# Performance work log

Hardware: AMD Instinct MI355X
Metric: run time of the kernel (lower is better)

## Reference

```python
import jax, jax.numpy as jnp
import numpy as np

N_NODES = 50000
N_EDGES = 800000
D = 128          # d_model
N_LAYER = 4
N_GRAPHS = 128
N_IDS = 256      # nn.Embedding(256, d_model)


def setup_inputs() -> dict:
    key = jax.random.key(0)
    ks = jax.random.split(key, 10)
    s = 0.02
    return {
        "position_feature": jax.random.normal(ks[0], (N_NODES, 3), dtype=jnp.float32),
        "id_feature": jax.random.randint(ks[1], (N_NODES,), 0, N_IDS),
        "edge_index": jax.random.randint(ks[2], (2, N_EDGES), 0, N_NODES),
        "batch": jnp.sort(jax.random.randint(ks[3], (N_NODES,), 0, N_GRAPHS)),
        "num_graphs": N_GRAPHS,
        "Wp": jax.random.normal(ks[4], (3, D), dtype=jnp.float32) * s,
        "bp": jnp.zeros((D,), jnp.float32),
        "id_emb": jax.random.normal(ks[5], (N_IDS, D), dtype=jnp.float32) * s,
        "Wn": jax.random.normal(ks[6], (2 * D, D), dtype=jnp.float32) * s,
        "bn": jnp.zeros((D,), jnp.float32),
        "conv_W": jax.random.normal(ks[7], (N_LAYER, D, D), dtype=jnp.float32) * s,
        "conv_b": jnp.zeros((N_LAYER, D), jnp.float32),
        "Wa": jax.random.normal(ks[8], ((1 + N_LAYER) * D, D), dtype=jnp.float32) * s,
        "ba": jnp.zeros((D,), jnp.float32),
    }


def _gcn(x, W, b, src, dst, norm, n):
    # PyG GCNConv: h = x @ W; out[dst] += norm(e) * h[src]; out += bias
    h = x @ W
    msg = h[src] * norm[:, None]
    return jax.ops.segment_sum(msg, dst, num_segments=n) + b


def reference(position_feature, id_feature, edge_index, batch, num_graphs,
              Wp, bp, id_emb, Wn, bn, conv_W, conv_b, Wa, ba):
    n = position_feature.shape[0]
    # GCN normalization with self-loops (shared across all layers)
    loops = jnp.arange(n)
    src = jnp.concatenate([edge_index[0], loops])
    dst = jnp.concatenate([edge_index[1], loops])
    deg = jax.ops.segment_sum(jnp.ones_like(src, dtype=position_feature.dtype), dst, num_segments=n)
    dinv = jnp.where(deg > 0, jax.lax.rsqrt(deg), 0.0)
    norm = dinv[src] * dinv[dst]  # [E + N]

    pos = jax.nn.relu(position_feature @ Wp + bp)       # [N, D]
    idf = jax.nn.relu(id_emb[id_feature])               # [N, D]
    x = jax.nn.relu(jnp.concatenate([pos, idf], axis=1) @ Wn + bn)  # [N, D]

    gs = [jax.ops.segment_max(x, batch, num_segments=num_graphs)]   # g_embed_0
    h = x
    for l in range(conv_W.shape[0]):
        h = jax.nn.relu(_gcn(h, conv_W[l], conv_b[l], src, dst, norm, n))
        gs.append(jax.ops.segment_max(h, batch, num_segments=num_graphs))

    g_embed = jnp.concatenate(gs, axis=1)  # [G, (1+n_layer)*D]
    return g_embed @ Wa + ba               # [G, D]
```

## Files before the change

### kernel.cpp

```cpp
#include <hip/hip_runtime.h>

#define N_NODES 50000
#define N_EDGES 800000
#define D 128
#define NLAYER 4
#define NGRAPH 128
#define GDIM (5 * D)
#define NBUCK 196

typedef __attribute__((ext_vector_type(8))) short bf16x8;
typedef __attribute__((ext_vector_type(4))) float f32x4;

__device__ __forceinline__ float b2f(unsigned short u) {
    return __uint_as_float(((unsigned)u) << 16);
}
__device__ __forceinline__ unsigned short f2b(float f) {
    unsigned u = __float_as_uint(f);
    unsigned r = (u + 0x7fffu + ((u >> 16) & 1u)) >> 16;
    return (unsigned short)r;
}


__global__ void k_count(const int* __restrict__ edst, int* __restrict__ cnt) {
    int e = blockIdx.x * 256 + threadIdx.x;
    if (e < N_EDGES) atomicAdd(&cnt[edst[e]], 1);
}

__global__ void k_scanA(const int* __restrict__ cnt, int* __restrict__ offs,
                        int* __restrict__ chunkSum) {
    __shared__ int lds[256];
    int tid = threadIdx.x;
    int base = blockIdx.x * 1024 + tid * 4;
    int v[4];
    int s = 0;
#pragma unroll
    for (int j = 0; j < 4; ++j) {
        int idx = base + j;
        v[j] = (idx < N_NODES) ? cnt[idx] : 0;
        s += v[j];
    }
    lds[tid] = s;
    __syncthreads();
    int t = s;
    for (int off = 1; off < 256; off <<= 1) {
        int add = (tid >= off) ? lds[tid - off] : 0;
        __syncthreads();
        t += add;
        lds[tid] = t;
        __syncthreads();
    }
    int run = t - s;
#pragma unroll
    for (int j = 0; j < 4; ++j) {
        int idx = base + j;
        if (idx < N_NODES) offs[idx] = run;
        run += v[j];
    }
    if (tid == 255) chunkSum[blockIdx.x] = t;
}

__global__ void k_scanB(const int* __restrict__ chunkSum, int* __restrict__ chunkOff,
                        int nc) {
    __shared__ int lds[64];
    int tid = threadIdx.x;
    int v = (tid < nc) ? chunkSum[tid] : 0;
    lds[tid] = v;
    __syncthreads();
    int t = v;
    for (int off = 1; off < 64; off <<= 1) {
        int add = (tid >= off) ? lds[tid - off] : 0;
        __syncthreads();
        t += add;
        lds[tid] = t;
        __syncthreads();
    }
    if (tid < nc) chunkOff[tid] = t - v;
}

__global__ void k_scanC(int* __restrict__ offs, const int* __restrict__ chunkOff,
                        const int* __restrict__ cnt, float* __restrict__ dinv,
                        int* __restrict__ btail, int* __restrict__ bstart) {
    int i = blockIdx.x * 256 + threadIdx.x;
    if (i < N_NODES) {
        int v = offs[i] + chunkOff[i >> 10];
        offs[i] = v;
        dinv[i] = 1.f / sqrtf((float)(cnt[i] + 1));
        if ((i & 255) == 0) { btail[i >> 8] = v; bstart[i >> 8] = v; }
        if (i == 0) bstart[NBUCK] = N_EDGES;
    }
}

__global__ __launch_bounds__(256) void k_bucket(
    const int* __restrict__ esrc, const int* __restrict__ edst,
    int* __restrict__ btail, int* __restrict__ ebuf) {
    __shared__ int hcnt[NBUCK];
    __shared__ int hbase[NBUCK];
    int t = threadIdx.x;
    for (int i = t; i < NBUCK; i += 256) hcnt[i] = 0;
    __syncthreads();
    int e0 = blockIdx.x * 2048 + t;
    int d[8], s[8];
#pragma unroll
    for (int i = 0; i < 8; ++i) {
        int e = e0 + i * 256;
        if (e < N_EDGES) {
            d[i] = edst[e];
            s[i] = esrc[e];
            atomicAdd(&hcnt[d[i] >> 8], 1);
        } else {
            d[i] = -1;
        }
    }
    __syncthreads();
    for (int i = t; i < NBUCK; i += 256) {
        int c = hcnt[i];
        hbase[i] = (c > 0) ? atomicAdd(&btail[i], c) : 0;
        hcnt[i] = 0;
    }
    __syncthreads();
#pragma unroll
    for (int i = 0; i < 8; ++i) {
        if (d[i] >= 0) {
            int b = d[i] >> 8;
            int p = atomicAdd(&hcnt[b], 1);
            ebuf[hbase[b] + p] = (s[i] & 0xffff) | ((d[i] & 255) << 16);
        }
    }
}

__global__ __launch_bounds__(256) void k_fillB(
    const int* __restrict__ ebuf, const int* __restrict__ bstart,
    const int* __restrict__ offs, const float* __restrict__ dinv,
    unsigned int* __restrict__ csrs) {
    __shared__ int loffs[256];
    __shared__ int lcnt[256];
    __shared__ float ldinv[256];
    int b = blockIdx.x, t = threadIdx.x;
    int nbase = b << 8;
    if (nbase + t < N_NODES) {
        loffs[t] = offs[nbase + t];
        ldinv[t] = dinv[nbase + t];
    }
    lcnt[t] = 0;
    __syncthreads();
    int s0 = bstart[b], s1 = bstart[b + 1];
    for (int i = s0 + t; i < s1; i += 256) {
        int pk = ebuf[i];
        int ld = (pk >> 16) & 255;
        int src = pk & 0xffff;
        float w = dinv[src] * ldinv[ld];
        int p = atomicAdd(&lcnt[ld], 1);
        csrs[loffs[ld] + p] = (unsigned)src | ((unsigned)f2b(w) << 16);
    }
}


__global__ __launch_bounds__(256) void k_prep(
    const float* __restrict__ Wn, const float* __restrict__ convW,
    unsigned short* __restrict__ Wpack,
    const float* __restrict__ id_emb, float* __restrict__ T) {
    int blk = blockIdx.x;
    if (blk < 320) {
        int tid = blk * 256 + threadIdx.x;
        int m = tid >> 14;
        int rem = tid & 16383;
        int ct = rem >> 11, kc = (rem >> 9) & 3, l = (rem >> 3) & 63, j = rem & 7;
        int k = kc * 32 + ((l >> 4) * 8) + j;
        int n = ct * 16 + (l & 15);
        const float* src = (m == 0) ? Wn : (convW + (size_t)(m - 1) * 16384);
        Wpack[tid] = f2b(src[k * 128 + n]);
    } else {
        int t = threadIdx.x;
        int d = t & 127;
        int r = (blk - 320) * 2 + (t >> 7);
        float acc = 0.f;
        for (int k = 0; k < 128; ++k)
            acc = fmaf(fmaxf(id_emb[r * 128 + k], 0.f), Wn[(128 + k) * 128 + d], acc);
        T[r * 128 + d] = acc;
    }
}


__global__ __launch_bounds__(256) void k_encoder(
    const float* __restrict__ pos, const int* __restrict__ idfeat,
    const float* __restrict__ Wp, const float* __restrict__ bp,
    const unsigned short* __restrict__ WpackE, const float* __restrict__ bn,
    const float* __restrict__ T, unsigned short* __restrict__ A16,
    const int* __restrict__ batch, float* __restrict__ gbuf) {
    __shared__ unsigned short feat[64 * 128];
    __shared__ float posl[192];
    __shared__ int bbat[64];
    int t = threadIdx.x;
    int base = blockIdx.x * 64;
    int avail = N_NODES - base;
    if (t < 192) {
        int idx = base * 3 + t;
        posl[t] = (idx < N_NODES * 3) ? pos[idx] : 0.f;
    }
    if (t < 64) bbat[t] = (base + t < N_NODES) ? batch[base + t] : -1;
    __syncthreads();
#pragma unroll
    for (int i = 0; i < 4; ++i) {
        int gid = t + i * 256;
        int row = gid >> 4, kg = gid & 15;
        unsigned short u[8];
        if (row < avail) {
            float p0 = posl[row * 3], p1 = posl[row * 3 + 1], p2 = posl[row * 3 + 2];
#pragma unroll
            for (int j = 0; j < 8; ++j) {
                int d = kg * 8 + j;
                float v = fmaf(p0, Wp[d], fmaf(p1, Wp[128 + d], fmaf(p2, Wp[256 + d], bp[d])));
                u[j] = f2b(fmaxf(v, 0.f));
            }
        } else {
#pragma unroll
            for (int j = 0; j < 8; ++j) u[j] = 0;
        }
        char* dst = (char*)feat + row * 256 + ((kg * 16) ^ ((row & 7) << 4));
        *(uint4*)dst = *(uint4*)u;
    }
    __syncthreads();
    int wid = t >> 6, l = t & 63;
    int r0 = wid * 16;
    f32x4 acc[8];
#pragma unroll
    for (int ct = 0; ct < 8; ++ct) acc[ct] = (f32x4){0.f, 0.f, 0.f, 0.f};
    const bf16x8* wp = (const bf16x8*)WpackE;
#pragma unroll
    for (int kc = 0; kc < 4; ++kc) {
        int row = r0 + (l & 15);
        const char* ap = (const char*)feat + row * 256 +
                         ((kc * 64 + ((l >> 4) * 16)) ^ ((row & 7) << 4));
        bf16x8 afrag = *(const bf16x8*)ap;
#pragma unroll
        for (int ct = 0; ct < 8; ++ct) {
            bf16x8 bfrag = wp[(ct * 4 + kc) * 64 + l];
            acc[ct] = __builtin_amdgcn_mfma_f32_16x16x32_bf16(afrag, bfrag, acc[ct], 0, 0, 0);
        }
    }
    int subrow = (l >> 4) * 4, col0 = l & 15;
    int ids[4];
#pragma unroll
    for (int i = 0; i < 4; ++i) {
        int node = base + r0 + subrow + i;
        ids[i] = (node < N_NODES) ? idfeat[node] : 0;
    }
    __syncthreads();
#pragma unroll
    for (int ct = 0; ct < 8; ++ct) {
        int col = ct * 16 + col0;
        float bcol = bn[col];
#pragma unroll
        for (int i = 0; i < 4; ++i) {
            int node = base + r0 + subrow + i;
            unsigned short ob = 0;
            if (node < N_NODES) {
                float v = acc[ct][i] + bcol + T[ids[i] * 128 + col];
                ob = f2b(fmaxf(v, 0.f));
                A16[(size_t)node * 128 + col] = ob;
            }
            feat[(r0 + subrow + i) * 128 + col] = ob;
        }
    }
    __syncthreads();
    if (t < 128) {
        int j = 0;
        while (j < 64) {
            int g = bbat[j];
            float m = b2f(feat[j * 128 + t]);
            int k = j + 1;
            while (k < 64 && bbat[k] == g) { m = fmaxf(m, b2f(feat[k * 128 + t])); ++k; }
            if (g >= 0) atomicMax((int*)&gbuf[g * GDIM + t], __float_as_int(m));
            j = k;
        }
    }
}


__global__ __launch_bounds__(512) void k_layer(
    const unsigned short* __restrict__ Hin, unsigned short* __restrict__ Hout,
    const unsigned short* __restrict__ WpackL,
    const int* __restrict__ offs, const int* __restrict__ cnt,
    const unsigned int* __restrict__ csrs, const float* __restrict__ dinv,
    const float* __restrict__ bias, const int* __restrict__ batch,
    float* __restrict__ gbuf, int goff) {
    __shared__ unsigned short hagg[16 * 128];
    __shared__ float smx[16][132];
    __shared__ int bb[16];
    int tid = threadIdx.x;
    int wave = tid >> 6, lane = tid & 63;
    int sub = lane >> 5, l = lane & 31;
    int row = wave * 2 + sub;
    int nbase = blockIdx.x * 16;
    int node = nbase + row;
    if (tid < 16) bb[tid] = batch[nbase + tid];

    int start = offs[node];
    int c = cnt[node];
    float di = dinv[node];
    float sw = di * di;
    const ushort4* B4 = (const ushort4*)Hin;
    ushort4 sv = B4[(size_t)node * 32 + l];
    float4 acc;
    acc.x = sw * b2f(sv.x);
    acc.y = sw * b2f(sv.y);
    acc.z = sw * b2f(sv.z);
    acc.w = sw * b2f(sv.w);
    int j = 0;
    for (; j + 8 <= c; j += 8) {
        unsigned pk[8];
        ushort4 v[8];
#pragma unroll
        for (int i = 0; i < 8; ++i) pk[i] = csrs[start + j + i];
#pragma unroll
        for (int i = 0; i < 8; ++i) v[i] = B4[(size_t)(pk[i] & 0xffffu) * 32 + l];
#pragma unroll
        for (int i = 0; i < 8; ++i) {
            float w = __uint_as_float(pk[i] & 0xffff0000u);
            acc.x = fmaf(w, b2f(v[i].x), acc.x);
            acc.y = fmaf(w, b2f(v[i].y), acc.y);
            acc.z = fmaf(w, b2f(v[i].z), acc.z);
            acc.w = fmaf(w, b2f(v[i].w), acc.w);
        }
    }
    for (; j < c; ++j) {
        unsigned pk = csrs[start + j];
        float w = __uint_as_float(pk & 0xffff0000u);
        ushort4 v = B4[(size_t)(pk & 0xffffu) * 32 + l];
        acc.x = fmaf(w, b2f(v.x), acc.x);
        acc.y = fmaf(w, b2f(v.y), acc.y);
        acc.z = fmaf(w, b2f(v.z), acc.z);
        acc.w = fmaf(w, b2f(v.w), acc.w);
    }
    {
        unsigned short u[4] = {f2b(acc.x), f2b(acc.y), f2b(acc.z), f2b(acc.w)};
        char* dst = (char*)hagg + row * 256 + ((((l >> 1) * 16) ^ ((row & 7) << 4)) + (l & 1) * 8);
        *(uint2*)dst = *(uint2*)u;
    }
    __syncthreads();

    f32x4 oacc = (f32x4){0.f, 0.f, 0.f, 0.f};
    const bf16x8* wp = (const bf16x8*)WpackL;
#pragma unroll
    for (int kc = 0; kc < 4; ++kc) {
        int arow = lane & 15;
        const char* ap = (const char*)hagg + arow * 256 +
                         ((kc * 64 + ((lane >> 4) * 16)) ^ ((arow & 7) << 4));
        bf16x8 afrag = *(const bf16x8*)ap;
        bf16x8 bfrag = wp[(wave * 4 + kc) * 64 + lane];
        oacc = __builtin_amdgcn_mfma_f32_16x16x32_bf16(afrag, bfrag, oacc, 0, 0, 0);
    }

    int col = wave * 16 + (lane & 15);
    int subrow = (lane >> 4) * 4;
    float bcol = bias[col];
#pragma unroll
    for (int i = 0; i < 4; ++i) {
        int r = subrow + i;
        float v = fmaxf(oacc[i] + bcol, 0.f);
        smx[r][col] = v;
        Hout[(size_t)(nbase + r) * 128 + col] = f2b(v);
    }
    __syncthreads();
    if (tid < 128) {
        int jj = 0;
        while (jj < 16) {
            int g = bb[jj];
            float m = smx[jj][tid];
            int k = jj + 1;
            while (k < 16 && bb[k] == g) { m = fmaxf(m, smx[k][tid]); ++k; }
            atomicMax((int*)&gbuf[g * GDIM + goff + tid], __float_as_int(m));
            jj = k;
        }
    }
}


__global__ __launch_bounds__(128) void k_final(const float* __restrict__ gbuf,
                                               const float* __restrict__ Wa,
                                               const float* __restrict__ ba,
                                               float* __restrict__ out) {
    __shared__ float gr[GDIM];
    int g = blockIdx.x, t = threadIdx.x;
    for (int i = t; i < GDIM; i += 128) gr[i] = gbuf[g * GDIM + i];
    __syncthreads();
    float acc = ba[t];
    for (int k = 0; k < GDIM; ++k) acc = fmaf(gr[k], Wa[k * 128 + t], acc);
    out[g * 128 + t] = acc;
}


extern "C" void kernel_launch(void* const* d_in, const int* in_sizes, int n_in,
                              void* d_out, int out_size, void* d_ws, size_t ws_size,
                              hipStream_t stream) {
    const float* pos    = (const float*)d_in[0];
    const int*   idfeat = (const int*)d_in[1];
    const int*   eidx   = (const int*)d_in[2];
    const int*   batch  = (const int*)d_in[3];
    const float* Wp     = (const float*)d_in[5];
    const float* bp     = (const float*)d_in[6];
    const float* id_emb = (const float*)d_in[7];
    const float* Wn     = (const float*)d_in[8];
    const float* bn     = (const float*)d_in[9];
    const float* convW  = (const float*)d_in[10];
    const float* convb  = (const float*)d_in[11];
    const float* Wa     = (const float*)d_in[12];
    const float* ba     = (const float*)d_in[13];
    float* out = (float*)d_out;

    const int* esrc = eidx;
    const int* edst = eidx + N_EDGES;

    char* w = (char*)d_ws;
    auto alloc = [&](size_t bytes) -> char* {
        char* p = w;
        w += (bytes + 255) & ~(size_t)255;
        return p;
    };
    int*   cnt  = (int*)alloc((size_t)N_NODES * 4);
    float* gbuf = (float*)alloc((size_t)NGRAPH * GDIM * 4);
    size_t zbytes = (((size_t)N_NODES * 4 + 255) & ~(size_t)255) + (size_t)NGRAPH * GDIM * 4;
    unsigned short* A16a = (unsigned short*)alloc((size_t)N_NODES * D * 2);
    unsigned short* A16b = (unsigned short*)alloc((size_t)N_NODES * D * 2);
    float* dinv = (float*)alloc((size_t)N_NODES * 4);
    int*   offs = (int*)alloc((size_t)(N_NODES + 1) * 4);
    int*   csum = (int*)alloc(64 * 4);
    int*   coff = (int*)alloc(64 * 4);
    unsigned int* csrs = (unsigned int*)alloc((size_t)N_EDGES * 4);
    int*   ebuf = (int*)alloc((size_t)N_EDGES * 4);
    int*   btail= (int*)alloc((NBUCK + 1) * 4);
    int*   bstart=(int*)alloc((NBUCK + 1) * 4);
    float* T    = (float*)alloc((size_t)256 * D * 4);
    unsigned short* Wpack = (unsigned short*)alloc((size_t)5 * 16384 * 2);

    hipMemsetAsync(cnt, 0, zbytes, stream);

    k_count<<<(N_EDGES + 255) / 256, 256, 0, stream>>>(edst, cnt);

    int nchunk = (N_NODES + 1023) / 1024;
    k_scanA<<<nchunk, 256, 0, stream>>>(cnt, offs, csum);
    k_scanB<<<1, 64, 0, stream>>>(csum, coff, nchunk);
    k_scanC<<<(N_NODES + 255) / 256, 256, 0, stream>>>(offs, coff, cnt, dinv, btail, bstart);

    k_bucket<<<(N_EDGES + 2047) / 2048, 256, 0, stream>>>(esrc, edst, btail, ebuf);
    k_fillB<<<NBUCK, 256, 0, stream>>>(ebuf, bstart, offs, dinv, csrs);

    k_prep<<<448, 256, 0, stream>>>(Wn, convW, Wpack, id_emb, T);
    k_encoder<<<(N_NODES + 63) / 64, 256, 0, stream>>>(pos, idfeat, Wp, bp, Wpack, bn, T,
                                                       A16a, batch, gbuf);

    unsigned short* Hin = A16a;
    unsigned short* Hout = A16b;
    for (int l = 0; l < NLAYER; ++l) {
        k_layer<<<N_NODES / 16, 512, 0, stream>>>(Hin, Hout, Wpack + (size_t)(l + 1) * 16384,
                                                  offs, cnt, csrs, dinv,
                                                  convb + (size_t)l * D, batch, gbuf,
                                                  (l + 1) * D);
        unsigned short* tmp = Hin; Hin = Hout; Hout = tmp;
    }

    k_final<<<NGRAPH, 128, 0, stream>>>(gbuf, Wa, ba, out);
}
```

Measured before the change: 298.9 us.

## Fuse degree count into bucketing and sort layer rows by graph and degree

Merges the degree-count kernel into the edge-bucketing pass by giving each bucket a fixed-capacity slot, so the bucketing no longer waits for the prefix scan. It also builds a node permutation keyed by (graph id, clamped degree) with a histogram, scan and scatter, and each layer block processes permuted nodes. Grouping nodes of similar degree is meant to even out per-wave gather work, and grouping by graph keeps the segment-max atomics merged within a block. The cost is indirect output writes, extra small kernels, and silent edge drops if a bucket ever exceeds its fixed capacity.

```diff
diff --git a/kernel.cpp b/kernel.cpp
--- a/kernel.cpp
+++ b/kernel.cpp
@@ -7,6 +7,7 @@
 #define NGRAPH 128
 #define GDIM (5 * D)
 #define NBUCK 196
+#define BCAP 4608
 
 typedef __attribute__((ext_vector_type(8))) short bf16x8;
 typedef __attribute__((ext_vector_type(4))) float f32x4;
@@ -21,10 +22,47 @@
 }
 
 
-__global__ void k_count(const int* __restrict__ edst, int* __restrict__ cnt) {
-    int e = blockIdx.x * 256 + threadIdx.x;
-    if (e < N_EDGES) atomicAdd(&cnt[edst[e]], 1);
-}
+__global__ __launch_bounds__(256) void k_bucket(
+    const int* __restrict__ esrc, const int* __restrict__ edst,
+    int* __restrict__ cnt, int* __restrict__ bcnt_rel, int* __restrict__ ebuf) {
+    __shared__ int hcnt[NBUCK];
+    __shared__ int hbase[NBUCK];
+    int t = threadIdx.x;
+    for (int i = t; i < NBUCK; i += 256) hcnt[i] = 0;
+    __syncthreads();
+    int e0 = blockIdx.x * 2048 + t;
+    int d[8], s[8];
+#pragma unroll
+    for (int i = 0; i < 8; ++i) {
+        int e = e0 + i * 256;
+        if (e < N_EDGES) {
+            d[i] = edst[e];
+            s[i] = esrc[e];
+            atomicAdd(&cnt[d[i]], 1);
+            atomicAdd(&hcnt[d[i] >> 8], 1);
+        } else {
+            d[i] = -1;
+        }
+    }
+    __syncthreads();
+    for (int i = t; i < NBUCK; i += 256) {
+        int c = hcnt[i];
+        hbase[i] = (c > 0) ? (i * BCAP + atomicAdd(&bcnt_rel[i], c)) : 0;
+        hcnt[i] = 0;
+    }
+    __syncthreads();
+#pragma unroll
+    for (int i = 0; i < 8; ++i) {
+        if (d[i] >= 0) {
+            int b = d[i] >> 8;
+            int p = atomicAdd(&hcnt[b], 1);
+            int pos = hbase[b] + p;
+            if (pos < (b + 1) * BCAP)
+                ebuf[pos] = (s[i] & 0xffff) | ((d[i] & 255) << 16);
+        }
+    }
+}
+
 
 __global__ void k_scanA(const int* __restrict__ cnt, int* __restrict__ offs,
                         int* __restrict__ chunkSum) {
@@ -79,57 +117,50 @@
 
 __global__ void k_scanC(int* __restrict__ offs, const int* __restrict__ chunkOff,
                         const int* __restrict__ cnt, float* __restrict__ dinv,
-                        int* __restrict__ btail, int* __restrict__ bstart) {
+                        const int* __restrict__ batch, int* __restrict__ hist2) {
     int i = blockIdx.x * 256 + threadIdx.x;
     if (i < N_NODES) {
-        int v = offs[i] + chunkOff[i >> 10];
-        offs[i] = v;
-        dinv[i] = 1.f / sqrtf((float)(cnt[i] + 1));
-        if ((i & 255) == 0) { btail[i >> 8] = v; bstart[i >> 8] = v; }
-        if (i == 0) bstart[NBUCK] = N_EDGES;
-    }
-}
-
-__global__ __launch_bounds__(256) void k_bucket(
-    const int* __restrict__ esrc, const int* __restrict__ edst,
-    int* __restrict__ btail, int* __restrict__ ebuf) {
-    __shared__ int hcnt[NBUCK];
-    __shared__ int hbase[NBUCK];
+        offs[i] += chunkOff[i >> 10];
+        int c = cnt[i];
+        dinv[i] = 1.f / sqrtf((float)(c + 1));
+        atomicAdd(&hist2[batch[i] * 128 + min(c, 127)], 1);
+    }
+}
+
+__global__ __launch_bounds__(1024) void k_scan16k(int* __restrict__ hist2) {
+    __shared__ int lds[1024];
     int t = threadIdx.x;
-    for (int i = t; i < NBUCK; i += 256) hcnt[i] = 0;
-    __syncthreads();
-    int e0 = blockIdx.x * 2048 + t;
-    int d[8], s[8];
-#pragma unroll
-    for (int i = 0; i < 8; ++i) {
-        int e = e0 + i * 256;
-        if (e < N_EDGES) {
-            d[i] = edst[e];
-            s[i] = esrc[e];
-            atomicAdd(&hcnt[d[i] >> 8], 1);
-        } else {
-            d[i] = -1;
-        }
-    }
-    __syncthreads();
-    for (int i = t; i < NBUCK; i += 256) {
-        int c = hcnt[i];
-        hbase[i] = (c > 0) ? atomicAdd(&btail[i], c) : 0;
-        hcnt[i] = 0;
-    }
-    __syncthreads();
-#pragma unroll
-    for (int i = 0; i < 8; ++i) {
-        if (d[i] >= 0) {
-            int b = d[i] >> 8;
-            int p = atomicAdd(&hcnt[b], 1);
-            ebuf[hbase[b] + p] = (s[i] & 0xffff) | ((d[i] & 255) << 16);
-        }
+    int v[16];
+    int s = 0;
+#pragma unroll
+    for (int j = 0; j < 16; ++j) { v[j] = hist2[t * 16 + j]; s += v[j]; }
+    lds[t] = s;
+    __syncthreads();
+    int tot = s;
+    for (int off = 1; off < 1024; off <<= 1) {
+        int add = (t >= off) ? lds[t - off] : 0;
+        __syncthreads();
+        tot += add;
+        lds[t] = tot;
+        __syncthreads();
+    }
+    int run = tot - s;
+#pragma unroll
+    for (int j = 0; j < 16; ++j) { hist2[t * 16 + j] = run; run += v[j]; }
+}
+
+__global__ void k_scatter(const int* __restrict__ cnt, const int* __restrict__ batch,
+                          int* __restrict__ hist2, int* __restrict__ perm) {
+    int i = blockIdx.x * 256 + threadIdx.x;
+    if (i < N_NODES) {
+        int key = batch[i] * 128 + min(cnt[i], 127);
+        int p = atomicAdd(&hist2[key], 1);
+        perm[p] = i;
     }
 }
 
 __global__ __launch_bounds__(256) void k_fillB(
-    const int* __restrict__ ebuf, const int* __restrict__ bstart,
+    const int* __restrict__ ebuf, const int* __restrict__ bcnt_rel,
     const int* __restrict__ offs, const float* __restrict__ dinv,
     unsigned int* __restrict__ csrs) {
     __shared__ int loffs[256];
@@ -143,7 +174,7 @@
     }
     lcnt[t] = 0;
     __syncthreads();
-    int s0 = bstart[b], s1 = bstart[b + 1];
+    int s0 = b * BCAP, s1 = b * BCAP + bcnt_rel[b];
     for (int i = s0 + t; i < s1; i += 256) {
         int pk = ebuf[i];
         int ld = (pk >> 16) & 255;
@@ -283,17 +314,22 @@
     const int* __restrict__ offs, const int* __restrict__ cnt,
     const unsigned int* __restrict__ csrs, const float* __restrict__ dinv,
     const float* __restrict__ bias, const int* __restrict__ batch,
-    float* __restrict__ gbuf, int goff) {
+    const int* __restrict__ perm, float* __restrict__ gbuf, int goff) {
     __shared__ unsigned short hagg[16 * 128];
     __shared__ float smx[16][132];
     __shared__ int bb[16];
+    __shared__ int snode[16];
     int tid = threadIdx.x;
     int wave = tid >> 6, lane = tid & 63;
     int sub = lane >> 5, l = lane & 31;
     int row = wave * 2 + sub;
     int nbase = blockIdx.x * 16;
-    int node = nbase + row;
-    if (tid < 16) bb[tid] = batch[nbase + tid];
+    if (tid < 16) {
+        int n = perm[nbase + tid];
+        snode[tid] = n;
+        bb[tid] = batch[n];
+    }
+    int node = perm[nbase + row];
 
     int start = offs[node];
     int c = cnt[node];
@@ -359,7 +395,7 @@
         int r = subrow + i;
         float v = fmaxf(oacc[i] + bcol, 0.f);
         smx[r][col] = v;
-        Hout[(size_t)(nbase + r) * 128 + col] = f2b(v);
+        Hout[(size_t)snode[r] * 128 + col] = f2b(v);
     }
     __syncthreads();
     if (tid < 128) {
@@ -417,9 +453,13 @@
         w += (bytes + 255) & ~(size_t)255;
         return p;
     };
-    int*   cnt  = (int*)alloc((size_t)N_NODES * 4);
-    float* gbuf = (float*)alloc((size_t)NGRAPH * GDIM * 4);
-    size_t zbytes = (((size_t)N_NODES * 4 + 255) & ~(size_t)255) + (size_t)NGRAPH * GDIM * 4;
+    char* zstart = w;
+    int*   cnt      = (int*)alloc((size_t)N_NODES * 4);
+    float* gbuf     = (float*)alloc((size_t)NGRAPH * GDIM * 4);
+    int*   hist2    = (int*)alloc((size_t)16384 * 4);
+    int*   bcnt_rel = (int*)alloc((size_t)NBUCK * 4);
+    size_t zbytes = (size_t)(w - zstart);
+
     unsigned short* A16a = (unsigned short*)alloc((size_t)N_NODES * D * 2);
     unsigned short* A16b = (unsigned short*)alloc((size_t)N_NODES * D * 2);
     float* dinv = (float*)alloc((size_t)N_NODES * 4);
@@ -427,23 +467,23 @@
     int*   csum = (int*)alloc(64 * 4);
     int*   coff = (int*)alloc(64 * 4);
     unsigned int* csrs = (unsigned int*)alloc((size_t)N_EDGES * 4);
-    int*   ebuf = (int*)alloc((size_t)N_EDGES * 4);
-    int*   btail= (int*)alloc((NBUCK + 1) * 4);
-    int*   bstart=(int*)alloc((NBUCK + 1) * 4);
+    int*   ebuf = (int*)alloc((size_t)NBUCK * BCAP * 4);
+    int*   perm = (int*)alloc((size_t)N_NODES * 4);
     float* T    = (float*)alloc((size_t)256 * D * 4);
     unsigned short* Wpack = (unsigned short*)alloc((size_t)5 * 16384 * 2);
 
-    hipMemsetAsync(cnt, 0, zbytes, stream);
-
-    k_count<<<(N_EDGES + 255) / 256, 256, 0, stream>>>(edst, cnt);
+    hipMemsetAsync(zstart, 0, zbytes, stream);
+
+    k_bucket<<<(N_EDGES + 2047) / 2048, 256, 0, stream>>>(esrc, edst, cnt, bcnt_rel, ebuf);
 
     int nchunk = (N_NODES + 1023) / 1024;
     k_scanA<<<nchunk, 256, 0, stream>>>(cnt, offs, csum);
     k_scanB<<<1, 64, 0, stream>>>(csum, coff, nchunk);
-    k_scanC<<<(N_NODES + 255) / 256, 256, 0, stream>>>(offs, coff, cnt, dinv, btail, bstart);
-
-    k_bucket<<<(N_EDGES + 2047) / 2048, 256, 0, stream>>>(esrc, edst, btail, ebuf);
-    k_fillB<<<NBUCK, 256, 0, stream>>>(ebuf, bstart, offs, dinv, csrs);
+    k_scanC<<<(N_NODES + 255) / 256, 256, 0, stream>>>(offs, coff, cnt, dinv, batch, hist2);
+    k_scan16k<<<1, 1024, 0, stream>>>(hist2);
+    k_scatter<<<(N_NODES + 255) / 256, 256, 0, stream>>>(cnt, batch, hist2, perm);
+
+    k_fillB<<<NBUCK, 256, 0, stream>>>(ebuf, bcnt_rel, offs, dinv, csrs);
 
     k_prep<<<448, 256, 0, stream>>>(Wn, convW, Wpack, id_emb, T);
     k_encoder<<<(N_NODES + 63) / 64, 256, 0, stream>>>(pos, idfeat, Wp, bp, Wpack, bn, T,
@@ -454,7 +494,7 @@
     for (int l = 0; l < NLAYER; ++l) {
         k_layer<<<N_NODES / 16, 512, 0, stream>>>(Hin, Hout, Wpack + (size_t)(l + 1) * 16384,
                                                   offs, cnt, csrs, dinv,
-                                                  convb + (size_t)l * D, batch, gbuf,
+                                                  convb + (size_t)l * D, batch, perm, gbuf,
                                                   (l + 1) * D);
         unsigned short* tmp = Hin; Hin = Hout; Hout = tmp;
     }
```

New measurement: 288.7 us. 1.04x faster.
